# Kernel optimization log

Measured on AMD Instinct MI355X. Metric: run time of the kernel, lower is better.

## Reference

```python
import jax, jax.numpy as jnp
import numpy as np

N_SAMPLES = 8_000_000
N_TRAIN = 1_000_000
KS = 9
HALF_KS = (KS - 1) // 2  # 4
SIGMA = 1.0


def _build_stats():
    """Replicates LDSLoss.__init__: histogramdd, gaussian LDS smoothing, scaling."""
    rng = np.random.default_rng(0)
    labels = rng.uniform(0.0, 10.0, size=(N_TRAIN, 2))
    n_bins = int((labels.max() - labels.min()) / 0.1)
    hist, edges = np.histogramdd(labels, bins=n_bins)
    # gaussian_filter1d(impulse, sigma)/max == exp(-0.5*(x/sigma)^2), truncated at 4*sigma (= half_ks)
    x = np.arange(-HALF_KS, HALF_KS + 1, dtype=np.float64)
    kernel = np.exp(-0.5 * (x / SIGMA) ** 2)
    # scipy.ndimage.convolve1d(hist, kernel, mode='constant') acts along the LAST axis only;
    # kernel is symmetric so convolution == correlation.
    pad = np.pad(hist, ((0, 0), (HALF_KS, HALF_KS)))
    smoothed = np.zeros_like(hist)
    for k in range(KS):
        smoothed += kernel[k] * pad[:, k:k + n_bins]
    bins0 = edges[0]
    bins1 = edges[1]
    # scaling = len(w)/sum(w) with w = 1/smoothed[bin(label)] over the training labels
    i0 = np.clip(np.searchsorted(bins0, labels[:, 0], side='right') - 1, 0, n_bins - 1)
    i1 = np.clip(np.searchsorted(bins1, labels[:, 1], side='right') - 1, 0, n_bins - 1)
    w = 1.0 / smoothed[i0, i1]
    scaling = len(w) / w.sum()
    lo = np.array([bins0[0], bins1[0]])
    hi = np.array([bins0[-1], bins1[-1]])
    return (smoothed.astype(np.float32), bins0.astype(np.float32),
            bins1.astype(np.float32), np.float32(scaling), lo, hi)


def setup_inputs() -> dict:
    smoothed, bins0, bins1, scaling, lo, hi = _build_stats()
    key = jax.random.key(0)
    k1, k2 = jax.random.split(key)
    inp = jax.random.normal(k1, (N_SAMPLES, 2), dtype=jnp.float32)
    # targets drawn inside the training-label range (as histogram bins cover it)
    tgt = jax.random.uniform(k2, (N_SAMPLES, 2), dtype=jnp.float32,
                             minval=jnp.asarray(lo, jnp.float32),
                             maxval=jnp.asarray(hi, jnp.float32))
    return {
        "input": inp,
        "target": tgt,
        "smoothed_distribution": jnp.asarray(smoothed),
        "bins0": jnp.asarray(bins0),
        "bins1": jnp.asarray(bins1),
        "scaling": jnp.asarray(scaling),
    }


def reference(input, target, smoothed_distribution, bins0, bins1, scaling):
    nb = smoothed_distribution.shape[0]
    # torch.where(label < bins)[0][0] - 1  ==  searchsorted(bins, label, 'right') - 1,
    # with the 'no edge greater' case mapped to the last bin (len(bins)-2).
    i0 = jnp.clip(jnp.searchsorted(bins0, target[:, 0], side='right') - 1, 0, nb - 1)
    i1 = jnp.clip(jnp.searchsorted(bins1, target[:, 1], side='right') - 1, 0, nb - 1)
    kernel_weights = smoothed_distribution[i0, i1]          # irregular gather  [N]
    weights = 1.0 / kernel_weights
    inf_mask = jnp.isinf(weights)
    finite_max = jnp.max(jnp.where(inf_mask, -jnp.inf, weights))
    weights = jnp.where(inf_mask, finite_max, weights) * scaling
    loss = (input - target) ** 2                             # MSELoss(reduction='none')
    loss = loss * weights[:, None]
    return jnp.mean(loss)
```

## Files before the change

kernel.cpp:

```cpp
#include <hip/hip_runtime.h>
#include <hip/hip_cooperative_groups.h>
#include <math.h>

namespace cg = cooperative_groups;


#define BLOCK 512
#define GRID_BLKS 512

__device__ __forceinline__ int find_bin(const float* __restrict__ sb, int nb,
                                        float x, float lo, float inv_step) {
    int g = (int)floorf((x - lo) * inv_step);
    g = g < 0 ? 0 : (g > nb - 1 ? nb - 1 : g);
    float e0 = sb[g];
    float e1 = sb[g + 1];
    g += (x >= e1) ? 1 : 0;
    g -= (x < e0) ? 1 : 0;
    return g < 0 ? 0 : (g > nb - 1 ? nb - 1 : g);
}

__device__ __forceinline__ void process_pair(
    float4 in, float4 tg,
    float* __restrict__ hist,
    const float* __restrict__ sb0, const float* __restrict__ sb1, int nb,
    float lo0, float inv0, float lo1, float inv1)
{
    float dA0 = in.x - tg.x, dA1 = in.y - tg.y;
    float sqA = dA0 * dA0 + dA1 * dA1;
    int iA0 = find_bin(sb0, nb, tg.x, lo0, inv0);
    int iA1 = find_bin(sb1, nb, tg.y, lo1, inv1);
    atomicAdd(&hist[iA0 * nb + iA1], sqA);

    float dB0 = in.z - tg.z, dB1 = in.w - tg.w;
    float sqB = dB0 * dB0 + dB1 * dB1;
    int iB0 = find_bin(sb0, nb, tg.z, lo0, inv0);
    int iB1 = find_bin(sb1, nb, tg.w, lo1, inv1);
    atomicAdd(&hist[iB0 * nb + iB1], sqB);
}

__global__ void __launch_bounds__(BLOCK)
lds_loss_coop(const float* __restrict__ input,
              const float* __restrict__ target,
              const float* __restrict__ smoothed,
              const float* __restrict__ bins0,
              const float* __restrict__ bins1,
              const float* __restrict__ scaling,
              int nb, long long n, long long nelem,
              double* __restrict__ partA,
              double* __restrict__ partB,
              float* __restrict__ partM,
              float* __restrict__ out)
{
    extern __shared__ __align__(16) float smem[];
    float* hist = smem;
    float* sb0  = smem + nb * nb;
    float* sb1  = sb0 + (nb + 1);

    const int nbnb = nb * nb;
    for (int i = threadIdx.x; i < nbnb; i += BLOCK) hist[i] = 0.0f;
    for (int i = threadIdx.x; i < nb + 1; i += BLOCK) {
        sb0[i] = bins0[i];
        sb1[i] = bins1[i];
    }
    __syncthreads();

    const float lo0 = sb0[0], inv0 = (float)nb / (sb0[nb] - sb0[0]);
    const float lo1 = sb1[0], inv1 = (float)nb / (sb1[nb] - sb1[0]);

    const long long npair = n >> 1;
    const float4* in4 = (const float4*)input;
    const float4* tg4 = (const float4*)target;
    const long long stride = (long long)gridDim.x * BLOCK;

    long long p = (long long)blockIdx.x * BLOCK + threadIdx.x;
    for (; p + 3 * stride < npair; p += 4 * stride) {
        float4 i0 = in4[p];
        float4 i1 = in4[p + stride];
        float4 i2 = in4[p + 2 * stride];
        float4 i3 = in4[p + 3 * stride];
        float4 t0 = tg4[p];
        float4 t1 = tg4[p + stride];
        float4 t2 = tg4[p + 2 * stride];
        float4 t3 = tg4[p + 3 * stride];
        process_pair(i0, t0, hist, sb0, sb1, nb, lo0, inv0, lo1, inv1);
        process_pair(i1, t1, hist, sb0, sb1, nb, lo0, inv0, lo1, inv1);
        process_pair(i2, t2, hist, sb0, sb1, nb, lo0, inv0, lo1, inv1);
        process_pair(i3, t3, hist, sb0, sb1, nb, lo0, inv0, lo1, inv1);
    }
    for (; p < npair; p += stride) {
        process_pair(in4[p], tg4[p], hist, sb0, sb1, nb, lo0, inv0, lo1, inv1);
    }

    if ((n & 1) && blockIdx.x == 0 && threadIdx.x == 0) {
        long long i = n - 1;
        float t0 = target[2 * i], t1 = target[2 * i + 1];
        float d0 = input[2 * i] - t0, d1 = input[2 * i + 1] - t1;
        float sq = d0 * d0 + d1 * d1;
        int j0 = find_bin(sb0, nb, t0, lo0, inv0);
        int j1 = find_bin(sb1, nb, t1, lo1, inv1);
        atomicAdd(&hist[j0 * nb + j1], sq);
    }
    __syncthreads();

    double A = 0.0, B = 0.0;
    float  m = 0.0f;
    for (int b = threadIdx.x; b < nbnb; b += BLOCK) {
        float h = hist[b];
        float s = smoothed[b];
        if (s == 0.0f) {
            B += (double)h;
        } else {
            float w = 1.0f / s;
            A += (double)w * (double)h;
            if (h > 0.0f) m = fmaxf(m, w);
        }
    }

    #pragma unroll
    for (int off = 32; off > 0; off >>= 1) {
        A += __shfl_down(A, off, 64);
        B += __shfl_down(B, off, 64);
        m = fmaxf(m, __shfl_down(m, off, 64));
    }

    __syncthreads();
    double* rA = (double*)smem;
    double* rB = rA + (BLOCK / 64);
    float*  rM = (float*)(rB + (BLOCK / 64));
    int wave = threadIdx.x >> 6;
    int lane = threadIdx.x & 63;
    if (lane == 0) { rA[wave] = A; rB[wave] = B; rM[wave] = m; }
    __syncthreads();
    if (threadIdx.x == 0) {
        double ta = 0.0, tb = 0.0; float tm = 0.0f;
        #pragma unroll
        for (int w2 = 0; w2 < BLOCK / 64; ++w2) {
            ta += rA[w2]; tb += rB[w2]; tm = fmaxf(tm, rM[w2]);
        }
        partA[blockIdx.x] = ta;
        partB[blockIdx.x] = tb;
        partM[blockIdx.x] = tm;
    }

    cg::this_grid().sync();

    if (blockIdx.x == 0) {
        int t = threadIdx.x;
        double a2 = (t < (int)gridDim.x) ? partA[t] : 0.0;
        double b2 = (t < (int)gridDim.x) ? partB[t] : 0.0;
        float  m2 = (t < (int)gridDim.x) ? partM[t] : 0.0f;
        #pragma unroll
        for (int off = 32; off > 0; off >>= 1) {
            a2 += __shfl_down(a2, off, 64);
            b2 += __shfl_down(b2, off, 64);
            m2 = fmaxf(m2, __shfl_down(m2, off, 64));
        }
        __syncthreads();
        if (lane == 0) { rA[wave] = a2; rB[wave] = b2; rM[wave] = m2; }
        __syncthreads();
        if (t == 0) {
            double ta = 0.0, tb = 0.0; float tm = 0.0f;
            #pragma unroll
            for (int w2 = 0; w2 < BLOCK / 64; ++w2) {
                ta += rA[w2]; tb += rB[w2]; tm = fmaxf(tm, rM[w2]);
            }
            double v = (double)(*scaling) * (ta + (double)tm * tb) / (double)nelem;
            *out = (float)v;
        }
    }
}

extern "C" void kernel_launch(void* const* d_in, const int* in_sizes, int n_in,
                              void* d_out, int out_size, void* d_ws, size_t ws_size,
                              hipStream_t stream) {
    const float* input    = (const float*)d_in[0];
    const float* target   = (const float*)d_in[1];
    const float* smoothed = (const float*)d_in[2];
    const float* bins0    = (const float*)d_in[3];
    const float* bins1    = (const float*)d_in[4];
    const float* scaling  = (const float*)d_in[5];

    long long nelem = in_sizes[0];
    long long n     = nelem / 2;
    int       nb    = in_sizes[3] - 1;

    double* partA = (double*)d_ws;
    double* partB = partA + GRID_BLKS;
    float*  partM = (float*)(partB + GRID_BLKS);
    float*  out   = (float*)d_out;

    unsigned int shmem =
        (unsigned int)(((size_t)nb * nb + 2 * (nb + 1)) * sizeof(float));

    void* args[] = {
        (void*)&input, (void*)&target, (void*)&smoothed,
        (void*)&bins0, (void*)&bins1, (void*)&scaling,
        (void*)&nb, (void*)&n, (void*)&nelem,
        (void*)&partA, (void*)&partB, (void*)&partM, (void*)&out
    };

    hipLaunchCooperativeKernel((void*)lds_loss_coop,
                               dim3(GRID_BLKS), dim3(BLOCK),
                               args, shmem, stream);
}
```

Before: 234.2 us.

## Replace cooperative grid sync with atomic last-block reduction and software-pipelined loads

The cooperative launch and grid-wide sync are replaced by a normal launch. Each block atomically adds its partial sums into global accumulators, and the last block to finish, detected with a done counter, writes the final result. The main loop is restructured into a double-buffered prefetch with sched_barriers so the next batch of float4 loads is in flight while the current pairs are binned. The block size grows to 1024. This aims to remove the cooperative launch and grid-sync overhead and to hide load latency, at the cost of an extra memset and double-precision global atomics.

```diff
diff --git a/kernel.cpp b/kernel.cpp
--- a/kernel.cpp
+++ b/kernel.cpp
@@ -1,11 +1,8 @@
 #include <hip/hip_runtime.h>
-#include <hip/hip_cooperative_groups.h>
 #include <math.h>
 
-namespace cg = cooperative_groups;
-
-
-#define BLOCK 512
+
+#define BLOCK 1024
 #define GRID_BLKS 512
 
 __device__ __forceinline__ int find_bin(const float* __restrict__ sb, int nb,
@@ -38,17 +35,18 @@
     atomicAdd(&hist[iB0 * nb + iB1], sqB);
 }
 
-__global__ void __launch_bounds__(BLOCK)
-lds_loss_coop(const float* __restrict__ input,
+__global__ void __launch_bounds__(BLOCK, 8)
+lds_loss_hist(const float* __restrict__ input,
               const float* __restrict__ target,
               const float* __restrict__ smoothed,
               const float* __restrict__ bins0,
               const float* __restrict__ bins1,
               const float* __restrict__ scaling,
               int nb, long long n, long long nelem,
-              double* __restrict__ partA,
-              double* __restrict__ partB,
-              float* __restrict__ partM,
+              double* __restrict__ accA,
+              double* __restrict__ accB,
+              unsigned int* __restrict__ accM,
+              unsigned int* __restrict__ done_ctr,
               float* __restrict__ out)
 {
     extern __shared__ __align__(16) float smem[];
@@ -70,25 +68,44 @@
     const long long npair = n >> 1;
     const float4* in4 = (const float4*)input;
     const float4* tg4 = (const float4*)target;
-    const long long stride = (long long)gridDim.x * BLOCK;
-
-    long long p = (long long)blockIdx.x * BLOCK + threadIdx.x;
-    for (; p + 3 * stride < npair; p += 4 * stride) {
-        float4 i0 = in4[p];
-        float4 i1 = in4[p + stride];
-        float4 i2 = in4[p + 2 * stride];
-        float4 i3 = in4[p + 3 * stride];
-        float4 t0 = tg4[p];
-        float4 t1 = tg4[p + stride];
-        float4 t2 = tg4[p + 2 * stride];
-        float4 t3 = tg4[p + 3 * stride];
-        process_pair(i0, t0, hist, sb0, sb1, nb, lo0, inv0, lo1, inv1);
-        process_pair(i1, t1, hist, sb0, sb1, nb, lo0, inv0, lo1, inv1);
-        process_pair(i2, t2, hist, sb0, sb1, nb, lo0, inv0, lo1, inv1);
-        process_pair(i3, t3, hist, sb0, sb1, nb, lo0, inv0, lo1, inv1);
-    }
-    for (; p < npair; p += stride) {
-        process_pair(in4[p], tg4[p], hist, sb0, sb1, nb, lo0, inv0, lo1, inv1);
+    const long long S = (long long)gridDim.x * BLOCK;
+    const long long STEP = 2 * S;
+
+    long long base = (long long)blockIdx.x * BLOCK + threadIdx.x;
+
+    float4 ai0, ai1, at0, at1;
+    float4 bi0, bi1, bt0, bt1;
+
+    bool haveA = (base + S) < npair;
+    if (haveA) {
+        ai0 = in4[base]; ai1 = in4[base + S];
+        at0 = tg4[base]; at1 = tg4[base + S];
+    }
+    while (haveA) {
+        long long nxtB = base + STEP;
+        bool haveB = (nxtB + S) < npair;
+        if (haveB) {
+            bi0 = in4[nxtB]; bi1 = in4[nxtB + S];
+            bt0 = tg4[nxtB]; bt1 = tg4[nxtB + S];
+        }
+        __builtin_amdgcn_sched_barrier(0);
+        process_pair(ai0, at0, hist, sb0, sb1, nb, lo0, inv0, lo1, inv1);
+        process_pair(ai1, at1, hist, sb0, sb1, nb, lo0, inv0, lo1, inv1);
+        if (!haveB) { base = nxtB; haveA = false; break; }
+
+        long long nxtA = nxtB + STEP;
+        haveA = (nxtA + S) < npair;
+        if (haveA) {
+            ai0 = in4[nxtA]; ai1 = in4[nxtA + S];
+            at0 = tg4[nxtA]; at1 = tg4[nxtA + S];
+        }
+        __builtin_amdgcn_sched_barrier(0);
+        process_pair(bi0, bt0, hist, sb0, sb1, nb, lo0, inv0, lo1, inv1);
+        process_pair(bi1, bt1, hist, sb0, sb1, nb, lo0, inv0, lo1, inv1);
+        base = nxtA;
+    }
+    for (long long r = base; r < npair; r += S) {
+        process_pair(in4[r], tg4[r], hist, sb0, sb1, nb, lo0, inv0, lo1, inv1);
     }
 
     if ((n & 1) && blockIdx.x == 0 && threadIdx.x == 0) {
@@ -107,10 +124,10 @@
     for (int b = threadIdx.x; b < nbnb; b += BLOCK) {
         float h = hist[b];
         float s = smoothed[b];
-        if (s == 0.0f) {
+        float w = 1.0f / s;
+        if (isinf(w)) {
             B += (double)h;
         } else {
-            float w = 1.0f / s;
             A += (double)w * (double)h;
             if (h > 0.0f) m = fmaxf(m, w);
         }
@@ -123,48 +140,29 @@
         m = fmaxf(m, __shfl_down(m, off, 64));
     }
 
-    __syncthreads();
-    double* rA = (double*)smem;
-    double* rB = rA + (BLOCK / 64);
-    float*  rM = (float*)(rB + (BLOCK / 64));
+    __shared__ double rA[BLOCK / 64], rB[BLOCK / 64];
+    __shared__ float  rM[BLOCK / 64];
     int wave = threadIdx.x >> 6;
     int lane = threadIdx.x & 63;
     if (lane == 0) { rA[wave] = A; rB[wave] = B; rM[wave] = m; }
     __syncthreads();
+
     if (threadIdx.x == 0) {
         double ta = 0.0, tb = 0.0; float tm = 0.0f;
         #pragma unroll
         for (int w2 = 0; w2 < BLOCK / 64; ++w2) {
             ta += rA[w2]; tb += rB[w2]; tm = fmaxf(tm, rM[w2]);
         }
-        partA[blockIdx.x] = ta;
-        partB[blockIdx.x] = tb;
-        partM[blockIdx.x] = tm;
-    }
-
-    cg::this_grid().sync();
-
-    if (blockIdx.x == 0) {
-        int t = threadIdx.x;
-        double a2 = (t < (int)gridDim.x) ? partA[t] : 0.0;
-        double b2 = (t < (int)gridDim.x) ? partB[t] : 0.0;
-        float  m2 = (t < (int)gridDim.x) ? partM[t] : 0.0f;
-        #pragma unroll
-        for (int off = 32; off > 0; off >>= 1) {
-            a2 += __shfl_down(a2, off, 64);
-            b2 += __shfl_down(b2, off, 64);
-            m2 = fmaxf(m2, __shfl_down(m2, off, 64));
-        }
-        __syncthreads();
-        if (lane == 0) { rA[wave] = a2; rB[wave] = b2; rM[wave] = m2; }
-        __syncthreads();
-        if (t == 0) {
-            double ta = 0.0, tb = 0.0; float tm = 0.0f;
-            #pragma unroll
-            for (int w2 = 0; w2 < BLOCK / 64; ++w2) {
-                ta += rA[w2]; tb += rB[w2]; tm = fmaxf(tm, rM[w2]);
-            }
-            double v = (double)(*scaling) * (ta + (double)tm * tb) / (double)nelem;
+        atomicAdd(accA, ta);
+        atomicAdd(accB, tb);
+        atomicMax(accM, __float_as_uint(tm));
+        __threadfence();
+        unsigned int prev = atomicAdd(done_ctr, 1u);
+        if (prev == gridDim.x - 1) {
+            double Af = atomicAdd(accA, 0.0);
+            double Bf = atomicAdd(accB, 0.0);
+            float  Mf = __uint_as_float(atomicMax(accM, 0u));
+            double v = (double)(*scaling) * (Af + (double)Mf * Bf) / (double)nelem;
             *out = (float)v;
         }
     }
@@ -180,26 +178,23 @@
     const float* bins1    = (const float*)d_in[4];
     const float* scaling  = (const float*)d_in[5];
 
-    long long nelem = in_sizes[0];
-    long long n     = nelem / 2;
-    int       nb    = in_sizes[3] - 1;
-
-    double* partA = (double*)d_ws;
-    double* partB = partA + GRID_BLKS;
-    float*  partM = (float*)(partB + GRID_BLKS);
-    float*  out   = (float*)d_out;
-
-    unsigned int shmem =
-        (unsigned int)(((size_t)nb * nb + 2 * (nb + 1)) * sizeof(float));
-
-    void* args[] = {
-        (void*)&input, (void*)&target, (void*)&smoothed,
-        (void*)&bins0, (void*)&bins1, (void*)&scaling,
-        (void*)&nb, (void*)&n, (void*)&nelem,
-        (void*)&partA, (void*)&partB, (void*)&partM, (void*)&out
-    };
-
-    hipLaunchCooperativeKernel((void*)lds_loss_coop,
-                               dim3(GRID_BLKS), dim3(BLOCK),
-                               args, shmem, stream);
-}
+    const long long nelem = in_sizes[0];
+    const long long n     = nelem / 2;
+    const int nb          = in_sizes[3] - 1;
+
+    double*       accA = (double*)d_ws;
+    double*       accB = accA + 1;
+    unsigned int* accM = (unsigned int*)(accB + 1);
+    unsigned int* ctr  = accM + 1;
+
+    hipMemsetAsync(d_ws, 0, 24, stream);
+
+    long long blocks_needed = (n / 2 + BLOCK - 1) / BLOCK;
+    int grid = (int)(blocks_needed < GRID_BLKS ? blocks_needed : GRID_BLKS);
+    if (grid < 1) grid = 1;
+    size_t shmem = ((size_t)nb * nb + 2 * (nb + 1)) * sizeof(float);
+
+    lds_loss_hist<<<grid, BLOCK, shmem, stream>>>(
+        input, target, smoothed, bins0, bins1, scaling,
+        nb, n, nelem, accA, accB, accM, ctr, (float*)d_out);
+}
```

New measurement: 188.7 us. 1.24x faster.
